# Kernel tuning notes

Hardware: AMD Instinct MI355X
Metric: run time of the kernel (lower is better)

Reference implementation:

```python
import jax, jax.numpy as jnp
import numpy as np
import math

IN_FEATURES = 1024
OUT_FEATURES = 1024
RANK = 16
ALPHA = 16.0
SCALING = ALPHA / RANK


def setup_inputs() -> dict:
    key = jax.random.key(0)
    k_x, k_w, k_b, k_a, k_bb = jax.random.split(key, 5)
    x = jax.random.normal(k_x, (8, 4096, IN_FEATURES), dtype=jnp.float32)
    # frozen linear params (W: [out, in], b: [out])
    W = jax.random.normal(k_w, (OUT_FEATURES, IN_FEATURES), dtype=jnp.float32) / math.sqrt(IN_FEATURES)
    b = jax.random.normal(k_b, (OUT_FEATURES,), dtype=jnp.float32) * 0.01
    # kaiming-uniform-like init for A; B nonzero here so the LoRA path is exercised
    bound = 1.0 / math.sqrt(IN_FEATURES)
    lora_A = jax.random.uniform(k_a, (RANK, IN_FEATURES), minval=-bound, maxval=bound, dtype=jnp.float32)
    lora_B = jax.random.normal(k_bb, (OUT_FEATURES, RANK), dtype=jnp.float32) * 0.02
    return {"x": x, "W": W, "b": b, "lora_A": lora_A, "lora_B": lora_B}


def reference(x, W, b, lora_A, lora_B):
    # y = x @ W^T + b + scaling * ((x @ A^T) @ B^T)
    # (mathematically identical to F.linear(x, B @ A); chained form avoids the
    #  full-rank [out, in] materialization)
    base = jnp.einsum("bsi,oi->bso", x, W) + b
    xa = jnp.einsum("bsi,ri->bsr", x, lora_A)      # [B, S, rank]
    lora_out = jnp.einsum("bsr,or->bso", xa, lora_B) * SCALING
    return base + lora_out
```

## Files before the change

kernel.cpp:

```cpp
#include <hip/hip_runtime.h>
#include <hip/hip_bf16.h>


typedef __bf16 bf16;
typedef bf16 bf16x8 __attribute__((ext_vector_type(8)));
typedef float f32x4 __attribute__((ext_vector_type(4)));

constexpr int K_DIM = 1024;
constexpr int N_DIM = 1024;
constexpr int M_DIM = 8 * 4096;
constexpr int NT = K_DIM / 64;
constexpr float SCALING = 16.0f / 16.0f;

__global__ __launch_bounds__(256) void weff_kernel(
    const float* __restrict__ W, const float* __restrict__ A,
    const float* __restrict__ B, bf16* __restrict__ weff) {
  const int o = blockIdx.x;
  const int tid = threadIdx.x;
  float br[16];
#pragma unroll
  for (int r = 0; r < 16; ++r) br[r] = B[o * 16 + r];
#pragma unroll
  for (int j = 0; j < 4; ++j) {
    const int k = tid + j * 256;
    float s = W[o * K_DIM + k];
#pragma unroll
    for (int r = 0; r < 16; ++r) s += SCALING * br[r] * A[r * K_DIM + k];
    weff[o * K_DIM + k] = (bf16)s;
  }
}

__device__ __forceinline__ void async16(const void* g, void* l) {
  __builtin_amdgcn_global_load_lds(
      (const __attribute__((address_space(1))) void*)g,
      (__attribute__((address_space(3))) void*)l, 16, 0, 0);
}
#define BAR() __builtin_amdgcn_s_barrier()
#define LGKM0()                                        \
  do {                                                 \
    asm volatile("s_waitcnt lgkmcnt(0)" ::: "memory"); \
    __builtin_amdgcn_sched_barrier(0);                 \
  } while (0)
#define VMW(n) asm volatile("s_waitcnt vmcnt(" #n ")" ::: "memory")
#define MFMA(d, a, b) d = __builtin_amdgcn_mfma_f32_16x16x32_bf16(a, b, d, 0, 0, 0)


__global__ __launch_bounds__(512, 2) void gemm8f(
    const float* __restrict__ Xf, const bf16* __restrict__ Wf,
    const float* __restrict__ bias, float* __restrict__ Y) {
  __shared__ __align__(16) bf16 smem[65536];

  const int tid = threadIdx.x;
  const int lane = tid & 63;
  const int wid = tid >> 6;
  const int wm = wid >> 2;
  const int wn = wid & 3;
  const int l15 = lane & 15;
  const int lq = lane >> 4;

  const int bid = blockIdx.x;
  const int wgid = (bid & 7) * 64 + (bid >> 3);
  const int bm = wgid >> 2;
  const int bn = wgid & 3;
  const long m0 = (long)bm * 256;
  const int n0 = bn * 256;

  const int srow = tid >> 3;
  const int gch = (tid & 7) ^ (srow & 7);
  const bf16* wsrc = Wf + (long)(n0 + srow) * K_DIM + gch * 8;
  auto stageB = [&](int tt, int h) {
    bf16* dst = smem + (tt & 1) * 32768 + 16384 + h * 8192 + tid * 8;
    const bf16* s = wsrc + (long)h * 128 * K_DIM + tt * 64;
    async16(s, dst);
    async16(s + 64 * K_DIM, dst + 4096);
  };

  const int arow = tid >> 2;
  const int acp = tid & 3;
  const int ar7 = arow & 7;
  const int aslot0 = (2 * acp) ^ ar7;
  const int aslot1 = (2 * acp + 1) ^ ar7;
  const float* asrc = Xf + (m0 + arow) * K_DIM + acp * 16;

  f32x4 rA0[4], rA1[4];
  auto loadA0 = [&](int tt) {
    const float* s = asrc + tt * 64;
#pragma unroll
    for (int i = 0; i < 4; ++i) rA0[i] = *(const f32x4*)(s + i * 4);
  };
  auto loadA1 = [&](int tt) {
    const float* s = asrc + (long)128 * K_DIM + tt * 64;
#pragma unroll
    for (int i = 0; i < 4; ++i) rA1[i] = *(const f32x4*)(s + i * 4);
  };
  auto writeA = [&](int tt, int h, f32x4* r) {
    bf16* dst = smem + (tt & 1) * 32768 + h * 8192 + arow * 64;
    bf16x8 c0, c1;
#pragma unroll
    for (int j = 0; j < 4; ++j) {
      c0[j] = (bf16)r[0][j];
      c0[4 + j] = (bf16)r[1][j];
      c1[j] = (bf16)r[2][j];
      c1[4 + j] = (bf16)r[3][j];
    }
    *(bf16x8*)(dst + aslot0 * 8) = c0;
    *(bf16x8*)(dst + aslot1 * 8) = c1;
  };

  const int key = l15 & 7;
  const int ck0 = lq ^ key;
  const int eA = (wm * 128 + l15) * 64 + ck0 * 8;
  const int eB = (wn * 64 + l15) * 64 + ck0 * 8;

  f32x4 acc[8][4] = {};

  stageB(0, 0); stageB(0, 1); stageB(1, 0); stageB(1, 1);
  loadA0(0); loadA1(0);
  writeA(0, 0, rA0); writeA(0, 1, rA1);
  loadA0(1); loadA1(1);
  writeA(1, 0, rA0); writeA(1, 1, rA1);
  VMW(0);
  asm volatile("s_waitcnt lgkmcnt(0)" ::: "memory");
  BAR();

  for (int t = 0; t < NT; ++t) {
    const bf16* Ab = smem + (t & 1) * 32768;
    const bf16* Bb = Ab + 16384;
    bf16x8 B0[4], B1[4];
    {
      bf16x8 A[4];
#pragma unroll
      for (int i = 0; i < 4; ++i) A[i] = *(const bf16x8*)(Ab + eA + i * 1024);
#pragma unroll
      for (int i = 0; i < 4; ++i) B0[i] = *(const bf16x8*)(Bb + eB + i * 1024);
      if (t < NT - 1) loadA0(t + 1);
      BAR();
      LGKM0();
      __builtin_amdgcn_s_setprio(1);
#pragma unroll
      for (int m = 0; m < 4; ++m)
#pragma unroll
        for (int n = 0; n < 4; ++n) MFMA(acc[m][n], A[m], B0[n]);
      __builtin_amdgcn_s_setprio(0);
      BAR();
    }
    {
      bf16x8 A[4];
#pragma unroll
      for (int i = 0; i < 4; ++i)
        A[i] = *(const bf16x8*)(Ab + (eA ^ 32) + i * 1024);
#pragma unroll
      for (int i = 0; i < 4; ++i)
        B1[i] = *(const bf16x8*)(Bb + (eB ^ 32) + i * 1024);
      if (t < NT - 1) loadA1(t + 1);
      BAR();
      LGKM0();
      __builtin_amdgcn_s_setprio(1);
#pragma unroll
      for (int m = 0; m < 4; ++m)
#pragma unroll
        for (int n = 0; n < 4; ++n) MFMA(acc[m][n], A[m], B1[n]);
      __builtin_amdgcn_s_setprio(0);
      BAR();
    }
    {
      bf16x8 A[4];
#pragma unroll
      for (int i = 0; i < 4; ++i)
        A[i] = *(const bf16x8*)(Ab + eA + 4096 + i * 1024);
      if (t < NT - 2) stageB(t + 2, 0);
      if (t < NT - 1) writeA(t + 1, 0, rA0);
      BAR();
      LGKM0();
      __builtin_amdgcn_s_setprio(1);
#pragma unroll
      for (int m = 0; m < 4; ++m)
#pragma unroll
        for (int n = 0; n < 4; ++n) MFMA(acc[4 + m][n], A[m], B0[n]);
      __builtin_amdgcn_s_setprio(0);
      BAR();
    }
    {
      bf16x8 A[4];
#pragma unroll
      for (int i = 0; i < 4; ++i)
        A[i] = *(const bf16x8*)(Ab + (eA ^ 32) + 4096 + i * 1024);
      if (t < NT - 2) stageB(t + 2, 1);
      if (t < NT - 1) writeA(t + 1, 1, rA1);
      BAR();
      LGKM0();
      __builtin_amdgcn_s_setprio(1);
#pragma unroll
      for (int m = 0; m < 4; ++m)
#pragma unroll
        for (int n = 0; n < 4; ++n) MFMA(acc[4 + m][n], A[m], B1[n]);
      __builtin_amdgcn_s_setprio(0);
      if (t < NT - 2) {
        VMW(4);
      } else {
        VMW(0);
      }
      BAR();
    }
  }

  const long crow0 = m0 + wm * 128 + lq * 4;
  const int ccol0 = n0 + wn * 64 + l15;
  float bn4[4];
#pragma unroll
  for (int n = 0; n < 4; ++n) bn4[n] = bias[ccol0 + n * 16];
#pragma unroll
  for (int m = 0; m < 8; ++m)
#pragma unroll
    for (int n = 0; n < 4; ++n) {
      const int col = ccol0 + n * 16;
#pragma unroll
      for (int i = 0; i < 4; ++i)
        Y[(crow0 + m * 16 + i) * N_DIM + col] = acc[m][n][i] + bn4[n];
    }
}

extern "C" void kernel_launch(void* const* d_in, const int* in_sizes, int n_in,
                              void* d_out, int out_size, void* d_ws, size_t ws_size,
                              hipStream_t stream) {
  const float* x = (const float*)d_in[0];
  const float* W = (const float*)d_in[1];
  const float* b = (const float*)d_in[2];
  const float* lA = (const float*)d_in[3];
  const float* lB = (const float*)d_in[4];
  float* y = (float*)d_out;

  bf16* weff = (bf16*)d_ws;

  weff_kernel<<<dim3(1024), dim3(256), 0, stream>>>(W, lA, lB, weff);

  const int grid = (M_DIM / 256) * (N_DIM / 256);
  gemm8f<<<dim3(grid), dim3(512), 0, stream>>>(x, weff, b, y);
}
```

Baseline: 119.7 us.

## Prefetch fp32 A tiles two iterations ahead with double-buffered registers

The fp32 X loads now fetch tile t+2 into one of two register sets that alternate between even and odd steps, and the loop is unrolled by two so the buffers can swap. Each global load therefore has a full tile iteration of MFMA work to hide its latency before it is converted and written to LDS. The vmcnt wait is relaxed to match the larger number of loads in flight. The cost is 32 more VGPRs for the second buffer set, which may press on occupancy under launch_bounds(512,2), plus changed prologue and epilogue handling.

```diff
diff --git a/kernel.cpp b/kernel.cpp
--- a/kernel.cpp
+++ b/kernel.cpp
@@ -82,18 +82,12 @@
   const int aslot1 = (2 * acp + 1) ^ ar7;
   const float* asrc = Xf + (m0 + arow) * K_DIM + acp * 16;
 
-  f32x4 rA0[4], rA1[4];
-  auto loadA0 = [&](int tt) {
-    const float* s = asrc + tt * 64;
-#pragma unroll
-    for (int i = 0; i < 4; ++i) rA0[i] = *(const f32x4*)(s + i * 4);
-  };
-  auto loadA1 = [&](int tt) {
-    const float* s = asrc + (long)128 * K_DIM + tt * 64;
-#pragma unroll
-    for (int i = 0; i < 4; ++i) rA1[i] = *(const f32x4*)(s + i * 4);
-  };
-  auto writeA = [&](int tt, int h, f32x4* r) {
+  auto loadAh = [&](int tt, int h, f32x4 (&r)[4]) {
+    const float* s = asrc + (long)h * 128 * K_DIM + tt * 64;
+#pragma unroll
+    for (int i = 0; i < 4; ++i) r[i] = *(const f32x4*)(s + i * 4);
+  };
+  auto writeA = [&](int tt, int h, f32x4 (&r)[4]) {
     bf16* dst = smem + (tt & 1) * 32768 + h * 8192 + arow * 64;
     bf16x8 c0, c1;
 #pragma unroll
@@ -114,16 +108,19 @@
 
   f32x4 acc[8][4] = {};
 
+  f32x4 s0h0[4], s0h1[4], s1h0[4], s1h1[4];
+
   stageB(0, 0); stageB(0, 1); stageB(1, 0); stageB(1, 1);
-  loadA0(0); loadA1(0);
-  writeA(0, 0, rA0); writeA(0, 1, rA1);
-  loadA0(1); loadA1(1);
-  writeA(1, 0, rA0); writeA(1, 1, rA1);
+  loadAh(0, 0, s0h0); loadAh(0, 1, s0h1);
+  writeA(0, 0, s0h0); writeA(0, 1, s0h1);
+  loadAh(1, 0, s0h0); loadAh(1, 1, s0h1);
+  writeA(1, 0, s0h0); writeA(1, 1, s0h1);
   VMW(0);
   asm volatile("s_waitcnt lgkmcnt(0)" ::: "memory");
   BAR();
 
-  for (int t = 0; t < NT; ++t) {
+  auto tile = [&](int t, f32x4 (&ld0)[4], f32x4 (&ld1)[4], f32x4 (&wr0)[4],
+                  f32x4 (&wr1)[4]) {
     const bf16* Ab = smem + (t & 1) * 32768;
     const bf16* Bb = Ab + 16384;
     bf16x8 B0[4], B1[4];
@@ -133,7 +130,7 @@
       for (int i = 0; i < 4; ++i) A[i] = *(const bf16x8*)(Ab + eA + i * 1024);
 #pragma unroll
       for (int i = 0; i < 4; ++i) B0[i] = *(const bf16x8*)(Bb + eB + i * 1024);
-      if (t < NT - 1) loadA0(t + 1);
+      if (t < NT - 2) loadAh(t + 2, 0, ld0);
       BAR();
       LGKM0();
       __builtin_amdgcn_s_setprio(1);
@@ -152,7 +149,7 @@
 #pragma unroll
       for (int i = 0; i < 4; ++i)
         B1[i] = *(const bf16x8*)(Bb + (eB ^ 32) + i * 1024);
-      if (t < NT - 1) loadA1(t + 1);
+      if (t < NT - 2) loadAh(t + 2, 1, ld1);
       BAR();
       LGKM0();
       __builtin_amdgcn_s_setprio(1);
@@ -169,7 +166,7 @@
       for (int i = 0; i < 4; ++i)
         A[i] = *(const bf16x8*)(Ab + eA + 4096 + i * 1024);
       if (t < NT - 2) stageB(t + 2, 0);
-      if (t < NT - 1) writeA(t + 1, 0, rA0);
+      if (t >= 1 && t < NT - 1) writeA(t + 1, 0, wr0);
       BAR();
       LGKM0();
       __builtin_amdgcn_s_setprio(1);
@@ -186,7 +183,7 @@
       for (int i = 0; i < 4; ++i)
         A[i] = *(const bf16x8*)(Ab + (eA ^ 32) + 4096 + i * 1024);
       if (t < NT - 2) stageB(t + 2, 1);
-      if (t < NT - 1) writeA(t + 1, 1, rA1);
+      if (t >= 1 && t < NT - 1) writeA(t + 1, 1, wr1);
       BAR();
       LGKM0();
       __builtin_amdgcn_s_setprio(1);
@@ -196,12 +193,17 @@
         for (int n = 0; n < 4; ++n) MFMA(acc[4 + m][n], A[m], B1[n]);
       __builtin_amdgcn_s_setprio(0);
       if (t < NT - 2) {
-        VMW(4);
-      } else {
+        VMW(12);
+      } else if (t == NT - 2) {
         VMW(0);
       }
       BAR();
     }
+  };
+
+  for (int t = 0; t < NT; t += 2) {
+    tile(t, s0h0, s0h1, s1h0, s1h1);
+    tile(t + 1, s1h0, s1h1, s0h0, s0h1);
   }
 
   const long crow0 = m0 + wm * 128 + lq * 4;
```

After: 232.4 us. 1.94x slower.

## Prefetch fp32 A tiles two iterations ahead to deepen global-load pipeline

Applied to the files above, without the earlier changes.

Moves the register prefetch of the fp32 X tile from one iteration ahead to two, so each global load has a full k-iteration to land before its bf16 conversion and LDS write. The vmcnt waits are adjusted to leave the newer A loads outstanding while only the B async copies are waited on. The aim is to hide global-memory latency on the fp32 activation stream, which dominates traffic. The prologue no longer writes tile 1 to LDS, since the loop now does that at t=0. The exact vmcnt counts must match the order in which loads are issued, so the change carries some correctness risk.

```diff
diff --git a/kernel.cpp b/kernel.cpp
--- a/kernel.cpp
+++ b/kernel.cpp
@@ -93,15 +93,28 @@
 #pragma unroll
     for (int i = 0; i < 4; ++i) rA1[i] = *(const f32x4*)(s + i * 4);
   };
-  auto writeA = [&](int tt, int h, f32x4* r) {
-    bf16* dst = smem + (tt & 1) * 32768 + h * 8192 + arow * 64;
+  auto writeA0 = [&](int tt) {
+    bf16* dst = smem + (tt & 1) * 32768 + arow * 64;
     bf16x8 c0, c1;
 #pragma unroll
     for (int j = 0; j < 4; ++j) {
-      c0[j] = (bf16)r[0][j];
-      c0[4 + j] = (bf16)r[1][j];
-      c1[j] = (bf16)r[2][j];
-      c1[4 + j] = (bf16)r[3][j];
+      c0[j] = (bf16)rA0[0][j];
+      c0[4 + j] = (bf16)rA0[1][j];
+      c1[j] = (bf16)rA0[2][j];
+      c1[4 + j] = (bf16)rA0[3][j];
+    }
+    *(bf16x8*)(dst + aslot0 * 8) = c0;
+    *(bf16x8*)(dst + aslot1 * 8) = c1;
+  };
+  auto writeA1 = [&](int tt) {
+    bf16* dst = smem + (tt & 1) * 32768 + 8192 + arow * 64;
+    bf16x8 c0, c1;
+#pragma unroll
+    for (int j = 0; j < 4; ++j) {
+      c0[j] = (bf16)rA1[0][j];
+      c0[4 + j] = (bf16)rA1[1][j];
+      c1[j] = (bf16)rA1[2][j];
+      c1[4 + j] = (bf16)rA1[3][j];
     }
     *(bf16x8*)(dst + aslot0 * 8) = c0;
     *(bf16x8*)(dst + aslot1 * 8) = c1;
@@ -114,12 +127,11 @@
 
   f32x4 acc[8][4] = {};
 
+  loadA0(0); loadA1(0);
   stageB(0, 0); stageB(0, 1); stageB(1, 0); stageB(1, 1);
-  loadA0(0); loadA1(0);
-  writeA(0, 0, rA0); writeA(0, 1, rA1);
+  writeA0(0); writeA1(0);
   loadA0(1); loadA1(1);
-  writeA(1, 0, rA0); writeA(1, 1, rA1);
-  VMW(0);
+  VMW(12);
   asm volatile("s_waitcnt lgkmcnt(0)" ::: "memory");
   BAR();
 
@@ -133,7 +145,6 @@
       for (int i = 0; i < 4; ++i) A[i] = *(const bf16x8*)(Ab + eA + i * 1024);
 #pragma unroll
       for (int i = 0; i < 4; ++i) B0[i] = *(const bf16x8*)(Bb + eB + i * 1024);
-      if (t < NT - 1) loadA0(t + 1);
       BAR();
       LGKM0();
       __builtin_amdgcn_s_setprio(1);
@@ -152,7 +163,6 @@
 #pragma unroll
       for (int i = 0; i < 4; ++i)
         B1[i] = *(const bf16x8*)(Bb + (eB ^ 32) + i * 1024);
-      if (t < NT - 1) loadA1(t + 1);
       BAR();
       LGKM0();
       __builtin_amdgcn_s_setprio(1);
@@ -169,7 +179,8 @@
       for (int i = 0; i < 4; ++i)
         A[i] = *(const bf16x8*)(Ab + eA + 4096 + i * 1024);
       if (t < NT - 2) stageB(t + 2, 0);
-      if (t < NT - 1) writeA(t + 1, 0, rA0);
+      if (t < NT - 1) writeA0(t + 1);
+      if (t < NT - 2) loadA0(t + 2);
       BAR();
       LGKM0();
       __builtin_amdgcn_s_setprio(1);
@@ -186,7 +197,8 @@
       for (int i = 0; i < 4; ++i)
         A[i] = *(const bf16x8*)(Ab + (eA ^ 32) + 4096 + i * 1024);
       if (t < NT - 2) stageB(t + 2, 1);
-      if (t < NT - 1) writeA(t + 1, 1, rA1);
+      if (t < NT - 1) writeA1(t + 1);
+      if (t < NT - 2) loadA1(t + 2);
       BAR();
       LGKM0();
       __builtin_amdgcn_s_setprio(1);
@@ -196,8 +208,8 @@
         for (int n = 0; n < 4; ++n) MFMA(acc[4 + m][n], A[m], B1[n]);
       __builtin_amdgcn_s_setprio(0);
       if (t < NT - 2) {
-        VMW(4);
-      } else {
+        VMW(12);
+      } else if (t == NT - 2) {
         VMW(0);
       }
       BAR();
```

Measured after the change: 117.8 us. About the same (-1.6%).
